# Kernel tuning notes

Hardware: AMD Instinct MI355X
Metric: run time of the kernel (lower is better)

## Reference

```python
import jax, jax.numpy as jnp
import numpy as np

D_TEXT, D_AUDIO, D_HID = 1024, 768, 1024
EPS = 1e-5


def layer_norm(x, gamma, beta):
    mu = jnp.mean(x, axis=-1, keepdims=True)
    var = jnp.mean(jnp.square(x - mu), axis=-1, keepdims=True)
    return (x - mu) * jax.lax.rsqrt(var + EPS) * gamma + beta


def setup_inputs() -> dict:
    key = jax.random.key(0)
    ks = jax.random.split(key, 8)
    B, L, S = 16, 1024, 2048
    # xavier_uniform bound = sqrt(6/(fan_in+fan_out))
    def xavier(k, shape):
        bound = np.sqrt(6.0 / (shape[0] + shape[1]))
        return jax.random.uniform(k, shape, jnp.float32, -bound, bound)
    return {
        "H_l": jax.random.normal(ks[0], (B, L, D_TEXT), jnp.float32),
        "H_a": jax.random.normal(ks[1], (B, S, D_AUDIO), jnp.float32),
        "W_text": xavier(ks[2], (D_TEXT, D_HID)),
        "b_text": jnp.zeros((D_HID,), jnp.float32),
        "W_audio": xavier(ks[3], (D_AUDIO, D_HID)),
        "b_audio": jnp.zeros((D_HID,), jnp.float32),
        "W_out": xavier(ks[4], (D_HID, D_HID)),
        "b_out": jnp.zeros((D_HID,), jnp.float32),
        "g1": jnp.ones((D_HID,), jnp.float32),
        "beta1": jnp.zeros((D_HID,), jnp.float32),
        "g2": jnp.ones((D_HID,), jnp.float32),
        "beta2": jnp.zeros((D_HID,), jnp.float32),
        "g_out": jnp.ones((D_HID,), jnp.float32),
        "beta_out": jnp.zeros((D_HID,), jnp.float32),
    }


def reference(H_l, H_a, W_text, b_text, W_audio, b_audio, W_out, b_out,
              g1, beta1, g2, beta2, g_out, beta_out):
    # projections
    text_p = jnp.einsum('bld,dh->blh', H_l, W_text) + b_text    # [B,L,H]
    audio_p = jnp.einsum('bsd,dh->bsh', H_a, W_audio) + b_audio  # [B,S,H]
    Q = layer_norm(text_p, g1, beta1)
    K = layer_norm(audio_p, g2, beta2)
    V = audio_p
    scale = 1.0 / np.sqrt(D_HID).astype(np.float32)
    scores = jnp.einsum('blh,bsh->bls', Q, K) * scale            # [B,L,S]
    alpha = jax.nn.softmax(scores, axis=-1)
    # dropout is identity in eval mode
    H_hyper = jnp.einsum('bls,bsh->blh', alpha, V)               # [B,L,H]
    H_hyper = jnp.einsum('blh,hk->blk', H_hyper, W_out) + b_out
    return layer_norm(H_hyper + H_l, g_out, beta_out)
```

## Files before the change

### kernel.cpp

```cpp
#include <hip/hip_runtime.h>
#include <cstdio>

typedef unsigned short u16;
typedef __bf16 bf16x8 __attribute__((ext_vector_type(8)));
typedef float f32x4 __attribute__((ext_vector_type(4)));
typedef unsigned short us4 __attribute__((ext_vector_type(4)));
typedef unsigned short us8 __attribute__((ext_vector_type(8)));

__device__ __forceinline__ u16 f2bf(float f) {
    union { float f; unsigned u; } x; x.f = f;
    unsigned u = x.u + 0x7fffu + ((x.u >> 16) & 1u);
    return (u16)(u >> 16);
}
__device__ __forceinline__ float bf2f(u16 u) {
    union { unsigned u; float f; } x; x.u = ((unsigned)u) << 16;
    return x.f;
}

template<int TAG, bool HAS_BIAS, bool HAS_RESID, bool OUT_BF16>
__global__ __launch_bounds__(512)
void gemm_nt(const u16* __restrict__ A, const u16* __restrict__ Bm,
             void* __restrict__ Cm, const float* __restrict__ bias,
             const float* __restrict__ resid,
             int K, int lda, int ldb, int ldc,
             long sA, long sB, long sC, float scale)
{
    __shared__ __align__(16) u16 lA[3][256 * 32];
    __shared__ __align__(16) u16 lB[3][256 * 32];

    const int tid = threadIdx.x;
    const long bz = blockIdx.z;
    A  += bz * sA;
    Bm += bz * sB;
    const long cbase = bz * sC;

    int bx, by;
    if (gridDim.z == 1) {
        const int gx = gridDim.x;
        const int flat = blockIdx.y * gx + blockIdx.x;
        const int q = (gx * gridDim.y) >> 3;
        const int wg = (flat & 7) * q + (flat >> 3);
        const int per = gx << 3;
        const int band = wg / per, rem = wg % per;
        bx = rem % gx;
        by = band * 8 + rem / gx;
    } else {
        bx = blockIdx.x; by = blockIdx.y;
    }
    const int m0 = by * 256;
    const int n0 = bx * 256;

    const int lane = tid & 63;
    const int w  = tid >> 6;
    const int wr = w >> 2, wc = w & 3;
    const int fr = lane & 15;
    const int kg = lane >> 4;

    f32x4 acc[8][4] = {};

    auto stage = [&](int b, int kt) {
#pragma unroll
        for (int h = 0; h < 2; ++h) {
            const int c = h * 512 + tid;
            const int row = c >> 2, seg = c & 3;
            const u16* sAp = A + (long)(m0 + row) * lda + (kt * 32 + seg * 8);
            __builtin_amdgcn_global_load_lds(
                (const __attribute__((address_space(1))) void*)sAp,
                (__attribute__((address_space(3))) void*)(&lA[b][c * 8]), 16, 0, 0);
            const u16* sBp = Bm + (long)(n0 + row) * ldb + (kt * 32 + seg * 8);
            __builtin_amdgcn_global_load_lds(
                (const __attribute__((address_space(1))) void*)sBp,
                (__attribute__((address_space(3))) void*)(&lB[b][c * 8]), 16, 0, 0);
        }
    };

    const int nk = K >> 5;
    stage(0, 0);
    stage(1, 1);
    for (int kt = 0; kt < nk; ++kt) {
        const int b = kt % 3;
        if (kt + 2 < nk) {
            stage((kt + 2) % 3, kt + 2);
            asm volatile("s_waitcnt vmcnt(8)" ::: "memory");
        } else if (kt + 1 < nk) {
            asm volatile("s_waitcnt vmcnt(4)" ::: "memory");
        } else {
            asm volatile("s_waitcnt vmcnt(0)" ::: "memory");
        }
        __builtin_amdgcn_s_barrier();
        asm volatile("" ::: "memory");

        bf16x8 af[8], bfv[4];
#pragma unroll
        for (int mf = 0; mf < 8; ++mf)
            af[mf] = *(const bf16x8*)&lA[b][(wr * 128 + mf * 16 + fr) * 32 + kg * 8];
#pragma unroll
        for (int nf = 0; nf < 4; ++nf)
            bfv[nf] = *(const bf16x8*)&lB[b][(wc * 64 + nf * 16 + fr) * 32 + kg * 8];

        __builtin_amdgcn_s_setprio(1);
#pragma unroll
        for (int mf = 0; mf < 8; ++mf)
#pragma unroll
            for (int nf = 0; nf < 4; ++nf)
                acc[mf][nf] = __builtin_amdgcn_mfma_f32_16x16x32_bf16(
                    af[mf], bfv[nf], acc[mf][nf], 0, 0, 0);
        __builtin_amdgcn_s_setprio(0);

        asm volatile("" ::: "memory");
        __builtin_amdgcn_s_barrier();
        asm volatile("" ::: "memory");
    }

    const int orow = m0 + wr * 128 + kg * 4;
    const int ocol = n0 + wc * 64 + fr;
#pragma unroll
    for (int mf = 0; mf < 8; ++mf) {
#pragma unroll
        for (int r = 0; r < 4; ++r) {
            const int m = orow + mf * 16 + r;
#pragma unroll
            for (int nf = 0; nf < 4; ++nf) {
                const int n = ocol + nf * 16;
                float v = acc[mf][nf][r] * scale;
                if (HAS_BIAS)  v += bias[n];
                if (HAS_RESID) v += resid[cbase + (long)m * ldc + n];
                if (OUT_BF16)  ((u16*)Cm)[cbase + (long)m * ldc + n] = f2bf(v);
                else           ((float*)Cm)[cbase + (long)m * ldc + n] = v;
            }
        }
    }
}

template<bool IN_BF16, bool OUT_BF16>
__global__ __launch_bounds__(256)
void ln1024(const void* in, const float* __restrict__ g,
            const float* __restrict__ beta, void* out)
{
    const long row = blockIdx.x;
    const int tid = threadIdx.x;
    float x0, x1, x2, x3;
    if (IN_BF16) {
        const us4 v = ((const us4*)in)[row * 256 + tid];
        x0 = bf2f(v[0]); x1 = bf2f(v[1]); x2 = bf2f(v[2]); x3 = bf2f(v[3]);
    } else {
        const float4 v = ((const float4*)in)[row * 256 + tid];
        x0 = v.x; x1 = v.y; x2 = v.z; x3 = v.w;
    }
    float s  = x0 + x1 + x2 + x3;
    float s2 = x0 * x0 + x1 * x1 + x2 * x2 + x3 * x3;
#pragma unroll
    for (int off = 32; off > 0; off >>= 1) {
        s  += __shfl_xor(s, off);
        s2 += __shfl_xor(s2, off);
    }
    __shared__ float rs[4], rq[4];
    if ((tid & 63) == 0) { rs[tid >> 6] = s; rq[tid >> 6] = s2; }
    __syncthreads();
    const float S  = rs[0] + rs[1] + rs[2] + rs[3];
    const float S2 = rq[0] + rq[1] + rq[2] + rq[3];
    const float mu = S * (1.0f / 1024.0f);
    const float var = S2 * (1.0f / 1024.0f) - mu * mu;
    const float rstd = rsqrtf(var + 1e-5f);
    const float4 gg = ((const float4*)g)[tid];
    const float4 bb = ((const float4*)beta)[tid];
    const float y0 = (x0 - mu) * rstd * gg.x + bb.x;
    const float y1 = (x1 - mu) * rstd * gg.y + bb.y;
    const float y2 = (x2 - mu) * rstd * gg.z + bb.z;
    const float y3 = (x3 - mu) * rstd * gg.w + bb.w;
    if (OUT_BF16) {
        us4 o; o[0] = f2bf(y0); o[1] = f2bf(y1); o[2] = f2bf(y2); o[3] = f2bf(y3);
        ((us4*)out)[row * 256 + tid] = o;
    } else {
        float4 o; o.x = y0; o.y = y1; o.z = y2; o.w = y3;
        ((float4*)out)[row * 256 + tid] = o;
    }
}

__global__ __launch_bounds__(256)
void softmax2048_bf16(u16* io)
{
    const long row = blockIdx.x;
    const int tid = threadIdx.x;
    const us8 v = ((const us8*)io)[row * 256 + tid];
    float x[8];
#pragma unroll
    for (int i = 0; i < 8; ++i) x[i] = bf2f(v[i]);
    float m = x[0];
#pragma unroll
    for (int i = 1; i < 8; ++i) m = fmaxf(m, x[i]);
#pragma unroll
    for (int off = 32; off > 0; off >>= 1) m = fmaxf(m, __shfl_xor(m, off));
    __shared__ float rm[4], rsum[4];
    if ((tid & 63) == 0) rm[tid >> 6] = m;
    __syncthreads();
    m = fmaxf(fmaxf(rm[0], rm[1]), fmaxf(rm[2], rm[3]));
    float e[8];
    float s = 0.f;
#pragma unroll
    for (int i = 0; i < 8; ++i) { e[i] = __expf(x[i] - m); s += e[i]; }
#pragma unroll
    for (int off = 32; off > 0; off >>= 1) s += __shfl_xor(s, off);
    if ((tid & 63) == 0) rsum[tid >> 6] = s;
    __syncthreads();
    s = rsum[0] + rsum[1] + rsum[2] + rsum[3];
    const float inv = 1.0f / s;
    us8 o;
#pragma unroll
    for (int i = 0; i < 8; ++i) o[i] = f2bf(e[i] * inv);
    ((us8*)io)[row * 256 + tid] = o;
}

__global__ __launch_bounds__(256)
void cast_f32_bf16(const float* __restrict__ in, u16* __restrict__ out, long n8)
{
    const long i = (long)blockIdx.x * 256 + threadIdx.x;
    if (i >= n8) return;
    const float4 a = ((const float4*)in)[i * 2];
    const float4 b = ((const float4*)in)[i * 2 + 1];
    us8 o;
    o[0] = f2bf(a.x); o[1] = f2bf(a.y); o[2] = f2bf(a.z); o[3] = f2bf(a.w);
    o[4] = f2bf(b.x); o[5] = f2bf(b.y); o[6] = f2bf(b.z); o[7] = f2bf(b.w);
    ((us8*)out)[i] = o;
}

__global__ __launch_bounds__(256)
void tcast_f32_bf16(const float* __restrict__ in, u16* __restrict__ out,
                    int R, int C)
{
    __shared__ float t[32][33];
    const int tx = threadIdx.x, ty = threadIdx.y;
    const int c0 = blockIdx.x * 32, r0 = blockIdx.y * 32;
#pragma unroll
    for (int i = 0; i < 4; ++i)
        t[ty + i * 8][tx] = in[(long)(r0 + ty + i * 8) * C + c0 + tx];
    __syncthreads();
#pragma unroll
    for (int i = 0; i < 4; ++i)
        out[(long)(c0 + ty + i * 8) * R + r0 + tx] = f2bf(t[tx][ty + i * 8]);
}

__global__ __launch_bounds__(256)
void t_bf16_batched(const u16* __restrict__ in, u16* __restrict__ out,
                    int R, int C)
{
    __shared__ u16 t[32][34];
    const int tx = threadIdx.x, ty = threadIdx.y;
    const int c0 = blockIdx.x * 32, r0 = blockIdx.y * 32;
    const long base = (long)blockIdx.z * R * C;
#pragma unroll
    for (int i = 0; i < 4; ++i)
        t[ty + i * 8][tx] = in[base + (long)(r0 + ty + i * 8) * C + c0 + tx];
    __syncthreads();
#pragma unroll
    for (int i = 0; i < 4; ++i)
        out[base + (long)(c0 + ty + i * 8) * R + r0 + tx] = t[tx][ty + i * 8];
}

extern "C" void kernel_launch(void* const* d_in, const int* in_sizes, int n_in,
                              void* d_out, int out_size, void* d_ws, size_t ws_size,
                              hipStream_t stream)
{
    const float* H_l      = (const float*)d_in[0];
    const float* H_a      = (const float*)d_in[1];
    const float* W_text   = (const float*)d_in[2];
    const float* b_text   = (const float*)d_in[3];
    const float* W_audio  = (const float*)d_in[4];
    const float* b_audio  = (const float*)d_in[5];
    const float* W_out    = (const float*)d_in[6];
    const float* b_out    = (const float*)d_in[7];
    const float* g1       = (const float*)d_in[8];
    const float* beta1    = (const float*)d_in[9];
    const float* g2       = (const float*)d_in[10];
    const float* beta2    = (const float*)d_in[11];
    const float* g_out    = (const float*)d_in[12];
    const float* beta_out = (const float*)d_in[13];
    (void)in_sizes; (void)n_in; (void)out_size;

    const int B = 16, L = 1024, S = 2048, DT = 1024, DA = 768, H = 1024;

    char* ws = (char*)d_ws;
    const size_t SZ_HLB = (size_t)B * L * DT * 2;
    const size_t SZ_HAB = (size_t)B * S * DA * 2;
    const size_t O_A    = SZ_HLB + SZ_HAB;
    const size_t SZ_A   = (size_t)B * L * H * 2;
    const size_t O_C    = O_A + SZ_A;
    const size_t SZ_C   = (size_t)B * S * H * 2;
    const size_t O_D    = O_C + SZ_C;
    const size_t SZ_D   = (size_t)B * S * H * 2;
    const size_t O_W    = O_D + SZ_D;
    const size_t need   = O_W + (size_t)(DT * H + DA * H + H * H) * 2;

    if (ws_size < need) {
        fprintf(stderr, "[kernel_launch] ws_size=%zu < needed=%zu — aborting launches\n",
                ws_size, need);
        return;
    }

    u16*   Hlb     = (u16*)(ws);
    u16*   Hab     = (u16*)(ws + SZ_HLB);
    u16*   Scores  = (u16*)(ws);
    u16*   Abuf    = (u16*)(ws + O_A);
    u16*   Vbuf    = (u16*)(ws + O_C);
    u16*   Kbuf    = (u16*)(ws + O_D);
    float* OutPre  = (float*)(ws + O_D);
    u16*   Wt_text  = (u16*)(ws + O_W);
    u16*   Wt_audio = Wt_text + (size_t)DT * H;
    u16*   Wt_out   = Wt_audio + (size_t)DA * H;
    u16*   Vt      = (u16*)d_out;

    const float scale = 0.03125f;

    cast_f32_bf16<<<(B * L * DT / 8 + 255) / 256, 256, 0, stream>>>(H_l, Hlb, (long)B * L * DT / 8);
    cast_f32_bf16<<<(B * S * DA / 8 + 255) / 256, 256, 0, stream>>>(H_a, Hab, (long)B * S * DA / 8);
    tcast_f32_bf16<<<dim3(H / 32, DT / 32), dim3(32, 8), 0, stream>>>(W_text, Wt_text, DT, H);
    tcast_f32_bf16<<<dim3(H / 32, DA / 32), dim3(32, 8), 0, stream>>>(W_audio, Wt_audio, DA, H);
    tcast_f32_bf16<<<dim3(H / 32, H / 32),  dim3(32, 8), 0, stream>>>(W_out, Wt_out, H, H);

    gemm_nt<1, true, false, true><<<dim3(H / 256, B * L / 256, 1), 512, 0, stream>>>(
        Hlb, Wt_text, Abuf, b_text, nullptr, DT, DT, DT, H, 0, 0, 0, 1.0f);
    ln1024<true, true><<<B * L, 256, 0, stream>>>(Abuf, g1, beta1, Abuf);

    gemm_nt<2, true, false, true><<<dim3(H / 256, B * S / 256, 1), 512, 0, stream>>>(
        Hab, Wt_audio, Vbuf, b_audio, nullptr, DA, DA, DA, H, 0, 0, 0, 1.0f);
    ln1024<true, true><<<B * S, 256, 0, stream>>>(Vbuf, g2, beta2, Kbuf);

    t_bf16_batched<<<dim3(H / 32, S / 32, B), dim3(32, 8), 0, stream>>>(Vbuf, Vt, S, H);

    gemm_nt<3, false, false, true><<<dim3(S / 256, L / 256, B), 512, 0, stream>>>(
        Abuf, Kbuf, Scores, nullptr, nullptr, H, H, H, S,
        (long)L * H, (long)S * H, (long)L * S, scale);

    softmax2048_bf16<<<B * L, 256, 0, stream>>>(Scores);

    gemm_nt<5, false, false, true><<<dim3(H / 256, L / 256, B), 512, 0, stream>>>(
        Scores, Vt, Abuf, nullptr, nullptr, S, S, S, H,
        (long)L * S, (long)H * S, (long)L * H, 1.0f);

    gemm_nt<6, true, true, false><<<dim3(H / 256, B * L / 256, 1), 512, 0, stream>>>(
        Abuf, Wt_out, OutPre, b_out, H_l, H, H, H, H, 0, 0, 0, 1.0f);

    ln1024<false, false><<<B * L, 256, 0, stream>>>(OutPre, g_out, beta_out, (float*)d_out);
}
```

Baseline: 588.9 us.

## Shrink GEMM tiles to 128x128, fuse V transpose into audio GEMM, bf16 pre-LN output

Every GEMM now uses 128x128 tiles with 256 threads in place of 256x256 tiles with 512 threads, and a unified grid swizzle also covers batched launches. The audio projection epilogue writes the transposed V directly, which removes the separate transpose kernel. The output projection now stores its pre-layernorm result in bf16 instead of fp32. Smaller tiles give more workgroups and better occupancy but less data reuse per tile, and the bf16 intermediate slightly reduces precision before the final layernorm.

```diff
diff --git a/kernel.cpp b/kernel.cpp
--- a/kernel.cpp
+++ b/kernel.cpp
@@ -17,51 +17,45 @@
     return x.f;
 }
 
-template<int TAG, bool HAS_BIAS, bool HAS_RESID, bool OUT_BF16>
-__global__ __launch_bounds__(512)
+template<int TAG, bool HAS_BIAS, bool HAS_RESID, bool OUT_BF16, bool EMIT_VT>
+__global__ __launch_bounds__(256)
 void gemm_nt(const u16* __restrict__ A, const u16* __restrict__ Bm,
              void* __restrict__ Cm, const float* __restrict__ bias,
-             const float* __restrict__ resid,
+             const float* __restrict__ resid, u16* __restrict__ vt,
              int K, int lda, int ldb, int ldc,
              long sA, long sB, long sC, float scale)
 {
-    __shared__ __align__(16) u16 lA[3][256 * 32];
-    __shared__ __align__(16) u16 lB[3][256 * 32];
+    __shared__ __align__(16) u16 lA[3][128 * 32];
+    __shared__ __align__(16) u16 lB[3][128 * 32];
 
     const int tid = threadIdx.x;
-    const long bz = blockIdx.z;
+
+    const int gx = gridDim.x, gy = gridDim.y;
+    int flat = ((int)blockIdx.z * gy + blockIdx.y) * gx + blockIdx.x;
+    const int nwg = gx * gy * (int)gridDim.z;
+    const int q = nwg >> 3;
+    flat = (flat & 7) * q + (flat >> 3);
+    const int bx = flat % gx;
+    const int t2 = flat / gx;
+    const int by = t2 % gy;
+    const long bz = t2 / gy;
+
     A  += bz * sA;
     Bm += bz * sB;
     const long cbase = bz * sC;
-
-    int bx, by;
-    if (gridDim.z == 1) {
-        const int gx = gridDim.x;
-        const int flat = blockIdx.y * gx + blockIdx.x;
-        const int q = (gx * gridDim.y) >> 3;
-        const int wg = (flat & 7) * q + (flat >> 3);
-        const int per = gx << 3;
-        const int band = wg / per, rem = wg % per;
-        bx = rem % gx;
-        by = band * 8 + rem / gx;
-    } else {
-        bx = blockIdx.x; by = blockIdx.y;
-    }
-    const int m0 = by * 256;
-    const int n0 = bx * 256;
+    const int m0 = by * 128;
+    const int n0 = bx * 128;
 
     const int lane = tid & 63;
     const int w  = tid >> 6;
-    const int wr = w >> 2, wc = w & 3;
+    const int wr = w >> 1, wc = w & 1;
     const int fr = lane & 15;
     const int kg = lane >> 4;
 
-    f32x4 acc[8][4] = {};
-
     auto stage = [&](int b, int kt) {
 #pragma unroll
         for (int h = 0; h < 2; ++h) {
-            const int c = h * 512 + tid;
+            const int c = h * 256 + tid;
             const int row = c >> 2, seg = c & 3;
             const u16* sAp = A + (long)(m0 + row) * lda + (kt * 32 + seg * 8);
             __builtin_amdgcn_global_load_lds(
@@ -73,6 +67,8 @@
                 (__attribute__((address_space(3))) void*)(&lB[b][c * 8]), 16, 0, 0);
         }
     };
+
+    f32x4 acc[4][4] = {};
 
     const int nk = K >> 5;
     stage(0, 0);
@@ -90,17 +86,17 @@
         __builtin_amdgcn_s_barrier();
         asm volatile("" ::: "memory");
 
-        bf16x8 af[8], bfv[4];
-#pragma unroll
-        for (int mf = 0; mf < 8; ++mf)
-            af[mf] = *(const bf16x8*)&lA[b][(wr * 128 + mf * 16 + fr) * 32 + kg * 8];
+        bf16x8 af[4], bfv[4];
+#pragma unroll
+        for (int mf = 0; mf < 4; ++mf)
+            af[mf] = *(const bf16x8*)&lA[b][(wr * 64 + mf * 16 + fr) * 32 + kg * 8];
 #pragma unroll
         for (int nf = 0; nf < 4; ++nf)
             bfv[nf] = *(const bf16x8*)&lB[b][(wc * 64 + nf * 16 + fr) * 32 + kg * 8];
 
         __builtin_amdgcn_s_setprio(1);
 #pragma unroll
-        for (int mf = 0; mf < 8; ++mf)
+        for (int mf = 0; mf < 4; ++mf)
 #pragma unroll
             for (int nf = 0; nf < 4; ++nf)
                 acc[mf][nf] = __builtin_amdgcn_mfma_f32_16x16x32_bf16(
@@ -112,21 +108,32 @@
         asm volatile("" ::: "memory");
     }
 
-    const int orow = m0 + wr * 128 + kg * 4;
+    const int orow = m0 + wr * 64 + kg * 4;
     const int ocol = n0 + wc * 64 + fr;
 #pragma unroll
-    for (int mf = 0; mf < 8; ++mf) {
-#pragma unroll
-        for (int r = 0; r < 4; ++r) {
-            const int m = orow + mf * 16 + r;
-#pragma unroll
-            for (int nf = 0; nf < 4; ++nf) {
-                const int n = ocol + nf * 16;
+    for (int mf = 0; mf < 4; ++mf) {
+        const int mbase = orow + mf * 16;
+#pragma unroll
+        for (int nf = 0; nf < 4; ++nf) {
+            const int n = ocol + nf * 16;
+            float v4[4];
+#pragma unroll
+            for (int r = 0; r < 4; ++r) {
+                const int m = mbase + r;
                 float v = acc[mf][nf][r] * scale;
                 if (HAS_BIAS)  v += bias[n];
                 if (HAS_RESID) v += resid[cbase + (long)m * ldc + n];
+                v4[r] = v;
                 if (OUT_BF16)  ((u16*)Cm)[cbase + (long)m * ldc + n] = f2bf(v);
                 else           ((float*)Cm)[cbase + (long)m * ldc + n] = v;
+            }
+            if (EMIT_VT) {
+                const long b_ = mbase >> 11;
+                const int  s  = mbase & 2047;
+                us4 o;
+#pragma unroll
+                for (int r = 0; r < 4; ++r) o[r] = f2bf(v4[r]);
+                *(us4*)(vt + (b_ * 1024 + n) * 2048 + s) = o;
             }
         }
     }
@@ -240,23 +247,6 @@
         out[(long)(c0 + ty + i * 8) * R + r0 + tx] = f2bf(t[tx][ty + i * 8]);
 }
 
-__global__ __launch_bounds__(256)
-void t_bf16_batched(const u16* __restrict__ in, u16* __restrict__ out,
-                    int R, int C)
-{
-    __shared__ u16 t[32][34];
-    const int tx = threadIdx.x, ty = threadIdx.y;
-    const int c0 = blockIdx.x * 32, r0 = blockIdx.y * 32;
-    const long base = (long)blockIdx.z * R * C;
-#pragma unroll
-    for (int i = 0; i < 4; ++i)
-        t[ty + i * 8][tx] = in[base + (long)(r0 + ty + i * 8) * C + c0 + tx];
-    __syncthreads();
-#pragma unroll
-    for (int i = 0; i < 4; ++i)
-        out[base + (long)(c0 + ty + i * 8) * R + r0 + tx] = t[tx][ty + i * 8];
-}
-
 extern "C" void kernel_launch(void* const* d_in, const int* in_sizes, int n_in,
                               void* d_out, int out_size, void* d_ws, size_t ws_size,
                               hipStream_t stream)
@@ -303,7 +293,7 @@
     u16*   Abuf    = (u16*)(ws + O_A);
     u16*   Vbuf    = (u16*)(ws + O_C);
     u16*   Kbuf    = (u16*)(ws + O_D);
-    float* OutPre  = (float*)(ws + O_D);
+    u16*   OutPre  = (u16*)(ws + O_D);
     u16*   Wt_text  = (u16*)(ws + O_W);
     u16*   Wt_audio = Wt_text + (size_t)DT * H;
     u16*   Wt_out   = Wt_audio + (size_t)DA * H;
@@ -317,28 +307,26 @@
     tcast_f32_bf16<<<dim3(H / 32, DA / 32), dim3(32, 8), 0, stream>>>(W_audio, Wt_audio, DA, H);
     tcast_f32_bf16<<<dim3(H / 32, H / 32),  dim3(32, 8), 0, stream>>>(W_out, Wt_out, H, H);
 
-    gemm_nt<1, true, false, true><<<dim3(H / 256, B * L / 256, 1), 512, 0, stream>>>(
-        Hlb, Wt_text, Abuf, b_text, nullptr, DT, DT, DT, H, 0, 0, 0, 1.0f);
+    gemm_nt<1, true, false, true, false><<<dim3(H / 128, B * L / 128, 1), 256, 0, stream>>>(
+        Hlb, Wt_text, Abuf, b_text, nullptr, nullptr, DT, DT, DT, H, 0, 0, 0, 1.0f);
     ln1024<true, true><<<B * L, 256, 0, stream>>>(Abuf, g1, beta1, Abuf);
 
-    gemm_nt<2, true, false, true><<<dim3(H / 256, B * S / 256, 1), 512, 0, stream>>>(
-        Hab, Wt_audio, Vbuf, b_audio, nullptr, DA, DA, DA, H, 0, 0, 0, 1.0f);
+    gemm_nt<2, true, false, true, true><<<dim3(H / 128, B * S / 128, 1), 256, 0, stream>>>(
+        Hab, Wt_audio, Vbuf, b_audio, nullptr, Vt, DA, DA, DA, H, 0, 0, 0, 1.0f);
     ln1024<true, true><<<B * S, 256, 0, stream>>>(Vbuf, g2, beta2, Kbuf);
 
-    t_bf16_batched<<<dim3(H / 32, S / 32, B), dim3(32, 8), 0, stream>>>(Vbuf, Vt, S, H);
-
-    gemm_nt<3, false, false, true><<<dim3(S / 256, L / 256, B), 512, 0, stream>>>(
-        Abuf, Kbuf, Scores, nullptr, nullptr, H, H, H, S,
+    gemm_nt<3, false, false, true, false><<<dim3(S / 128, L / 128, B), 256, 0, stream>>>(
+        Abuf, Kbuf, Scores, nullptr, nullptr, nullptr, H, H, H, S,
         (long)L * H, (long)S * H, (long)L * S, scale);
 
     softmax2048_bf16<<<B * L, 256, 0, stream>>>(Scores);
 
-    gemm_nt<5, false, false, true><<<dim3(H / 256, L / 256, B), 512, 0, stream>>>(
-        Scores, Vt, Abuf, nullptr, nullptr, S, S, S, H,
+    gemm_nt<5, false, false, true, false><<<dim3(H / 128, L / 128, B), 256, 0, stream>>>(
+        Scores, Vt, Abuf, nullptr, nullptr, nullptr, S, S, S, H,
         (long)L * S, (long)H * S, (long)L * H, 1.0f);
 
-    gemm_nt<6, true, true, false><<<dim3(H / 256, B * L / 256, 1), 512, 0, stream>>>(
-        Abuf, Wt_out, OutPre, b_out, H_l, H, H, H, H, 0, 0, 0, 1.0f);
-
-    ln1024<false, false><<<B * L, 256, 0, stream>>>(OutPre, g_out, beta_out, (float*)d_out);
-}
+    gemm_nt<6, true, true, true, false><<<dim3(H / 128, B * L / 128, 1), 256, 0, stream>>>(
+        Abuf, Wt_out, OutPre, b_out, H_l, nullptr, H, H, H, H, 0, 0, 0, 1.0f);
+
+    ln1024<true, false><<<B * L, 256, 0, stream>>>(OutPre, g_out, beta_out, (float*)d_out);
+}
```

After: 595.1 us. No clear change (+1.1%).
